# Performance work log

Measured on AMD Instinct MI355X. Metric: run time of the kernel, lower is better.

Reference implementation:

```python
import jax, jax.numpy as jnp
import numpy as np

N_NODES = 100000


def gcn_conv(x, edge_index, W, b):
    # PyG GCNConv: add self-loops, symmetric normalization D^-1/2 (A+I) D^-1/2, transform, aggregate, bias.
    src, dst = edge_index[0], edge_index[1]
    n = x.shape[0]
    xw = x @ W  # [N, out] transform before propagate (PyG order)
    # degree with self-loops (count edges by target + 1)
    deg = jax.ops.segment_sum(jnp.ones_like(dst, dtype=xw.dtype), dst, num_segments=n) + 1.0
    dinv = jax.lax.rsqrt(deg)  # deg >= 1, safe
    norm = dinv[src] * dinv[dst]  # [E]
    msgs = xw[src] * norm[:, None]  # [E, out] gathered, normalized messages
    agg = jax.ops.segment_sum(msgs, dst, num_segments=n)
    # self-loop contribution: norm_ii = dinv_i^2 = 1/deg_i
    agg = agg + xw * (dinv * dinv)[:, None]
    return agg + b


def setup_inputs() -> dict:
    key = jax.random.key(0)
    ks = jax.random.split(key, 8)
    in_c, h1, h2, out_c = 128, 71, 82, 1
    x = jax.random.normal(ks[0], (N_NODES, in_c), dtype=jnp.float32)
    edge_index = jax.random.randint(ks[1], (2, 1600000), 0, N_NODES, dtype=jnp.int64)
    def glorot(k, fan_in, fan_out):
        s = jnp.sqrt(6.0 / (fan_in + fan_out))
        return jax.random.uniform(k, (fan_in, fan_out), jnp.float32, -s, s)
    return {
        "x": x,
        "edge_index": edge_index,
        "W1": glorot(ks[2], in_c, h1), "b1": jnp.zeros((h1,), jnp.float32),
        "W2": glorot(ks[3], h1, h2), "b2": jnp.zeros((h2,), jnp.float32),
        "W3": glorot(ks[4], h2, out_c), "b3": jnp.zeros((out_c,), jnp.float32),
    }


def reference(x, edge_index, W1, b1, W2, b2, W3, b3):
    h = jax.nn.relu(gcn_conv(x, edge_index, W1, b1))
    h = gcn_conv(h, edge_index, W2, b2)  # note: no relu after conv2 in source
    return gcn_conv(h, edge_index, W3, b3)
```

## Files before the change

### kernel.cpp

```cpp
#include <hip/hip_runtime.h>
#include <hip/hip_fp16.h>

#define NNODES 100000
#define NB 196
#define BSHIFT 9
#define BMASK 511
#define BCAP 9216
#define WT_LD 136

typedef _Float16 half8 __attribute__((ext_vector_type(8)));
typedef float floatx4 __attribute__((ext_vector_type(4)));

__global__ void binA_kernel(const int* __restrict__ src, const int* __restrict__ dst,
                            int* __restrict__ bcnt, unsigned* __restrict__ bdata, int E) {
    __shared__ int hist[NB];
    __shared__ int gb[NB];
    __shared__ int cur[NB];
    const int BATCH = 4096;
    for (int base = blockIdx.x * BATCH; base < E; base += gridDim.x * BATCH) {
        for (int i = threadIdx.x; i < NB; i += blockDim.x) hist[i] = 0;
        __syncthreads();
        int s[16], d[16];
        int cnt = 0;
        if (base + BATCH <= E) {
#pragma unroll
            for (int q = 0; q < 4; ++q) {
                int4 sv = ((const int4*)(src + base))[q * 256 + threadIdx.x];
                int4 dv = ((const int4*)(dst + base))[q * 256 + threadIdx.x];
                s[cnt] = sv.x; d[cnt] = dv.x; atomicAdd(&hist[dv.x >> BSHIFT], 1); ++cnt;
                s[cnt] = sv.y; d[cnt] = dv.y; atomicAdd(&hist[dv.y >> BSHIFT], 1); ++cnt;
                s[cnt] = sv.z; d[cnt] = dv.z; atomicAdd(&hist[dv.z >> BSHIFT], 1); ++cnt;
                s[cnt] = sv.w; d[cnt] = dv.w; atomicAdd(&hist[dv.w >> BSHIFT], 1); ++cnt;
            }
        } else {
#pragma unroll
            for (int k = 0; k < 16; ++k) {
                int idx = base + k * 256 + threadIdx.x;
                if (idx < E) {
                    s[cnt] = src[idx];
                    d[cnt] = dst[idx];
                    atomicAdd(&hist[d[cnt] >> BSHIFT], 1);
                    ++cnt;
                }
            }
        }
        __syncthreads();
        for (int i = threadIdx.x; i < NB; i += blockDim.x) {
            int c = hist[i];
            gb[i] = (c > 0) ? atomicAdd(&bcnt[i], c) : 0;
            cur[i] = 0;
        }
        __syncthreads();
        for (int k = 0; k < cnt; ++k) {
            int b = d[k] >> BSHIFT;
            int lo = gb[b] + atomicAdd(&cur[b], 1);
            if (lo < BCAP)
                bdata[(size_t)b * BCAP + lo] = ((unsigned)s[k] << BSHIFT) | ((unsigned)d[k] & BMASK);
        }
        __syncthreads();
    }
}

__global__ void bscan_kernel(const int* __restrict__ bcnt, int* __restrict__ bstart) {
    __shared__ int sh[NB];
    int t = threadIdx.x;
    if (t < NB) sh[t] = min(bcnt[t], BCAP);
    __syncthreads();
    if (t == 0) {
        int acc = 0;
        for (int i = 0; i < NB; ++i) { int v = sh[i]; sh[i] = acc; acc += v; }
    }
    __syncthreads();
    if (t < NB) bstart[t] = sh[t];
}

__global__ __launch_bounds__(1024) void binB2_kernel(
        const int* __restrict__ bcnt, const int* __restrict__ bstart,
        const unsigned* __restrict__ bdata,
        int* __restrict__ deg, int* __restrict__ end_off, float* __restrict__ dinv,
        int* __restrict__ csr, int n) {
    __shared__ unsigned edata[BCAP];
    __shared__ int hist[512];
    __shared__ int cur[512];
    __shared__ int wsum[8];
    int b = blockIdx.x;
    int tid = threadIdx.x;
    int cnt = min(bcnt[b], BCAP);
    int base = bstart[b];
    const unsigned* p = bdata + (size_t)b * BCAP;
    if (tid < 512) hist[tid] = 0;
    __syncthreads();
    for (int i = tid; i < cnt; i += 1024) {
        unsigned e = p[i];
        edata[i] = e;
        atomicAdd(&hist[e & BMASK], 1);
    }
    __syncthreads();
    if (tid < 512) {
        int v = hist[tid];
        int lane = tid & 63;
        int incl = v;
#pragma unroll
        for (int off = 1; off < 64; off <<= 1) {
            int t = __shfl_up(incl, off);
            if (lane >= off) incl += t;
        }
        cur[tid] = incl;
        if (lane == 63) wsum[tid >> 6] = incl;
    }
    __syncthreads();
    if (tid == 0) {
        int acc = 0;
#pragma unroll
        for (int w = 0; w < 8; ++w) { int t = wsum[w]; wsum[w] = acc; acc += t; }
    }
    __syncthreads();
    if (tid < 512) {
        int v = hist[tid];
        int start = base + wsum[tid >> 6] + cur[tid] - v;
        int node = (b << BSHIFT) + tid;
        if (node < n) {
            deg[node] = v;
            end_off[node] = start + v;
            dinv[node] = rsqrtf((float)v + 1.0f);
        }
        cur[tid] = start;
    }
    __syncthreads();
    for (int i = tid; i < cnt; i += 1024) {
        unsigned e = edata[i];
        int pos = atomicAdd(&cur[e & BMASK], 1);
        csr[pos] = (int)(e >> BSHIFT);
    }
}

__global__ void w23_kernel(const float* __restrict__ W2, const float* __restrict__ b2,
                           const float* __restrict__ W3, float* __restrict__ w23) {
    int k = threadIdx.x;
    if (k < 71) {
        float a = 0.f;
        for (int j = 0; j < 82; ++j) a += W2[k * 82 + j] * W3[j];
        w23[k] = a;
    } else if (k == 71) {
        float a = 0.f;
        for (int j = 0; j < 82; ++j) a += b2[j] * W3[j];
        w23[71] = a;
    }
}

__global__ void wt_kernel(const float* __restrict__ W1, __half* __restrict__ Wt) {
    for (int i = threadIdx.x; i < 80 * WT_LD; i += blockDim.x) {
        int nn = i / WT_LD, k = i - nn * WT_LD;
        float v = (nn < 71 && k < 128) ? W1[k * 71 + nn] : 0.f;
        Wt[i] = __float2half(v);
    }
}

__global__ __launch_bounds__(256) void xform_mfma(
        const float* __restrict__ x, const __half* __restrict__ Wt,
        const float* __restrict__ scale, __half* __restrict__ msg, int n) {
    __shared__ __half Wsh[80 * WT_LD];
    {
        const uint4* sp = (const uint4*)Wt;
        uint4* dp = (uint4*)Wsh;
        for (int i = threadIdx.x; i < (80 * WT_LD * 2) / 16; i += blockDim.x) dp[i] = sp[i];
    }
    __syncthreads();
    int lane = threadIdx.x & 63;
    int m = lane & 15, q = lane >> 4;
    int gw = (blockIdx.x * blockDim.x + threadIdx.x) >> 6;
    int nw = (gridDim.x * blockDim.x) >> 6;
    int nrt = n >> 4;
    for (int rt = gw; rt < nrt; rt += nw) {
        int rb = rt << 4;
        const float* xr = x + (size_t)(rb + m) * 128 + q * 8;
        floatx4 acc[5];
#pragma unroll
        for (int t = 0; t < 5; ++t) acc[t] = (floatx4){0.f, 0.f, 0.f, 0.f};
#pragma unroll
        for (int ks = 0; ks < 4; ++ks) {
            float4 f0 = *(const float4*)(xr + ks * 32);
            float4 f1 = *(const float4*)(xr + ks * 32 + 4);
            half8 a;
            a[0] = (_Float16)f0.x; a[1] = (_Float16)f0.y;
            a[2] = (_Float16)f0.z; a[3] = (_Float16)f0.w;
            a[4] = (_Float16)f1.x; a[5] = (_Float16)f1.y;
            a[6] = (_Float16)f1.z; a[7] = (_Float16)f1.w;
#pragma unroll
            for (int t = 0; t < 5; ++t) {
                half8 b = *(const half8*)&Wsh[(t * 16 + m) * WT_LD + ks * 32 + q * 8];
                acc[t] = __builtin_amdgcn_mfma_f32_16x16x32_f16(a, b, acc[t], 0, 0, 0);
            }
        }
        float sc[4];
#pragma unroll
        for (int r = 0; r < 4; ++r) sc[r] = scale[rb + q * 4 + r];
#pragma unroll
        for (int t = 0; t < 5; ++t) {
            int col = t * 16 + m;
            if (col < 72) {
#pragma unroll
                for (int r = 0; r < 4; ++r)
                    msg[(size_t)(rb + q * 4 + r) * 72 + col] = __float2half(acc[t][r] * sc[r]);
            }
        }
    }
}

template <int OC>
__global__ void gather_fused(const __half2* __restrict__ msg, const int* __restrict__ csr,
                             const int* __restrict__ end_off, const int* __restrict__ deg,
                             const float* __restrict__ dinv, const float* __restrict__ b,
                             const float* __restrict__ w23, float* __restrict__ g2, int n) {
    constexpr int OC2 = (OC + 1) / 2;
    int lane = threadIdx.x & 63;
    int wid = (blockIdx.x * blockDim.x + threadIdx.x) >> 6;
    int nwaves = (gridDim.x * blockDim.x) >> 6;
    bool act = lane < OC2;
    int c = lane << 1;
    float bx = (act && c < OC) ? b[c] : 0.f;
    float by = (act && c + 1 < OC) ? b[c + 1] : 0.f;
    float w0 = (act && c < OC) ? w23[c] : 0.f;
    float w1 = (act && c + 1 < OC) ? w23[c + 1] : 0.f;
    for (int node = wid; node < n; node += nwaves) {
        int end = end_off[node];
        int cnt = deg[node];
        int start = end - cnt;
        float ax0 = 0.f, ay0 = 0.f, ax1 = 0.f, ay1 = 0.f;
        float ax2 = 0.f, ay2 = 0.f, ax3 = 0.f, ay3 = 0.f;
        for (int base = 0; base < cnt; base += 64) {
            int rem = min(cnt - base, 64);
            int se = (lane < rem) ? csr[start + base + lane] : 0;
            int j = 0;
            for (; j + 7 < rem; j += 8) {
                int s0 = __shfl(se, j),     s1 = __shfl(se, j + 1);
                int s2 = __shfl(se, j + 2), s3 = __shfl(se, j + 3);
                int s4 = __shfl(se, j + 4), s5 = __shfl(se, j + 5);
                int s6 = __shfl(se, j + 6), s7 = __shfl(se, j + 7);
                if (act) {
                    float2 v0 = __half22float2(msg[(size_t)s0 * OC2 + lane]);
                    float2 v1 = __half22float2(msg[(size_t)s1 * OC2 + lane]);
                    float2 v2 = __half22float2(msg[(size_t)s2 * OC2 + lane]);
                    float2 v3 = __half22float2(msg[(size_t)s3 * OC2 + lane]);
                    float2 v4 = __half22float2(msg[(size_t)s4 * OC2 + lane]);
                    float2 v5 = __half22float2(msg[(size_t)s5 * OC2 + lane]);
                    float2 v6 = __half22float2(msg[(size_t)s6 * OC2 + lane]);
                    float2 v7 = __half22float2(msg[(size_t)s7 * OC2 + lane]);
                    ax0 += v0.x; ay0 += v0.y;  ax1 += v1.x; ay1 += v1.y;
                    ax2 += v2.x; ay2 += v2.y;  ax3 += v3.x; ay3 += v3.y;
                    ax0 += v4.x; ay0 += v4.y;  ax1 += v5.x; ay1 += v5.y;
                    ax2 += v6.x; ay2 += v6.y;  ax3 += v7.x; ay3 += v7.y;
                }
            }
            for (; j + 3 < rem; j += 4) {
                int s0 = __shfl(se, j),     s1 = __shfl(se, j + 1);
                int s2 = __shfl(se, j + 2), s3 = __shfl(se, j + 3);
                if (act) {
                    float2 v0 = __half22float2(msg[(size_t)s0 * OC2 + lane]);
                    float2 v1 = __half22float2(msg[(size_t)s1 * OC2 + lane]);
                    float2 v2 = __half22float2(msg[(size_t)s2 * OC2 + lane]);
                    float2 v3 = __half22float2(msg[(size_t)s3 * OC2 + lane]);
                    ax0 += v0.x; ay0 += v0.y;  ax1 += v1.x; ay1 += v1.y;
                    ax2 += v2.x; ay2 += v2.y;  ax3 += v3.x; ay3 += v3.y;
                }
            }
            for (; j < rem; ++j) {
                int s = __shfl(se, j);
                if (act) {
                    float2 v = __half22float2(msg[(size_t)s * OC2 + lane]);
                    ax0 += v.x; ay0 += v.y;
                }
            }
        }
        float dv = dinv[node];
        float p = 0.f;
        if (act) {
            float2 selfv = __half22float2(msg[(size_t)node * OC2 + lane]);
            float sx = ((ax0 + ax1) + (ax2 + ax3)) + selfv.x;
            float sy = ((ay0 + ay1) + (ay2 + ay3)) + selfv.y;
            float vx = fmaxf(dv * sx + bx, 0.f);
            float vy = fmaxf(dv * sy + by, 0.f);
            p = vx * w0 + vy * w1;
        }
#pragma unroll
        for (int off = 32; off > 0; off >>= 1) p += __shfl_down(p, off);
        if (lane == 0) g2[node] = dv * p;
    }
}

__global__ void sgather_q(const float* __restrict__ g2, const int* __restrict__ csr,
                          const int* __restrict__ end_off, const int* __restrict__ deg,
                          const float* __restrict__ dinv, const float* __restrict__ w23,
                          float* __restrict__ q, int n) {
    float bw = w23[71];
    int stride = gridDim.x * blockDim.x;
    for (int i = blockIdx.x * blockDim.x + threadIdx.x; i < n; i += stride) {
        int end = end_off[i];
        int cnt = deg[i];
        float acc = 0.f;
        for (int j = end - cnt; j < end; ++j) acc += g2[csr[j]];
        float dv = dinv[i];
        q[i] = dv * (dv * (acc + g2[i]) + bw);
    }
}

__global__ void sgather_out(const float* __restrict__ q, const int* __restrict__ csr,
                            const int* __restrict__ end_off, const int* __restrict__ deg,
                            const float* __restrict__ dinv, const float* __restrict__ b3,
                            float* __restrict__ out, int n) {
    int stride = gridDim.x * blockDim.x;
    for (int i = blockIdx.x * blockDim.x + threadIdx.x; i < n; i += stride) {
        int end = end_off[i];
        int cnt = deg[i];
        float acc = 0.f;
        for (int j = end - cnt; j < end; ++j) acc += q[csr[j]];
        out[i] = dinv[i] * (acc + q[i]) + b3[0];
    }
}

extern "C" void kernel_launch(void* const* d_in, const int* in_sizes, int n_in,
                              void* d_out, int out_size, void* d_ws, size_t ws_size,
                              hipStream_t stream) {
    const float* x  = (const float*)d_in[0];
    const int*   ei = (const int*)d_in[1];
    const float* W1 = (const float*)d_in[2];
    const float* b1 = (const float*)d_in[3];
    const float* W2 = (const float*)d_in[4];
    const float* b2 = (const float*)d_in[5];
    const float* W3 = (const float*)d_in[6];
    const float* b3 = (const float*)d_in[7];
    float* out = (float*)d_out;

    const int n = NNODES;
    const int E = in_sizes[1] / 2;
    const int* src = ei;
    const int* dst = ei + E;

    float* ws     = (float*)d_ws;
    float* dinv   = ws;
    int*   deg_i  = (int*)(ws + n);
    int*   offs   = deg_i + n;
    int*   bcnt   = offs + n;
    int*   bstart = bcnt + 256;
    float* w23    = (float*)(bstart + 256);
    __half* Wt    = (__half*)(w23 + 80);
    float* g2     = (float*)(Wt + 11008);
    float* q      = g2 + n;
    int*   csr    = (int*)(q + n);
    __half* msg   = (__half*)(csr + E);
    unsigned* bdata = (unsigned*)(msg + (size_t)n * 72);

    hipMemsetAsync(bcnt, 0, 256 * sizeof(int), stream);
    binA_kernel<<<(E + 4095) / 4096, 256, 0, stream>>>(src, dst, bcnt, bdata, E);
    bscan_kernel<<<1, 256, 0, stream>>>(bcnt, bstart);
    binB2_kernel<<<NB, 1024, 0, stream>>>(bcnt, bstart, bdata, deg_i, offs, dinv, csr, n);
    w23_kernel<<<1, 128, 0, stream>>>(W2, b2, W3, w23);
    wt_kernel<<<1, 1024, 0, stream>>>(W1, Wt);

    xform_mfma<<<1563, 256, 0, stream>>>(x, Wt, dinv, msg, n);

    gather_fused<71><<<2048, 256, 0, stream>>>((const __half2*)msg, csr, offs, deg_i, dinv, b1, w23, g2, n);

    sgather_q<<<(n + 255) / 256, 256, 0, stream>>>(g2, csr, offs, deg_i, dinv, w23, q, n);
    sgather_out<<<(n + 255) / 256, 256, 0, stream>>>(q, csr, offs, deg_i, dinv, b3, out, n);
}
```

Baseline: 249.5 us.

## Gather multiple edges per wave with 16-byte loads and merge prep kernels

Rewrites the first-layer gather so each wave splits into 7 slots of 9 lanes. Each lane loads 8 fp16 features per edge with one vector load, so 7 neighbor rows are fetched concurrently instead of one row using 36 lanes. The self-loop is folded into the edge list, and partial sums are reduced across slots with shuffles. Separately, the bucket scan, the W2·W3 product and the W1 transpose kernels are merged into one 3-block launch to cut launch overhead. The cost is extra shuffle reductions and some idle lanes on low-degree tails.

```diff
diff --git a/kernel.cpp b/kernel.cpp
--- a/kernel.cpp
+++ b/kernel.cpp
@@ -61,17 +61,40 @@
     }
 }
 
-__global__ void bscan_kernel(const int* __restrict__ bcnt, int* __restrict__ bstart) {
-    __shared__ int sh[NB];
-    int t = threadIdx.x;
-    if (t < NB) sh[t] = min(bcnt[t], BCAP);
-    __syncthreads();
-    if (t == 0) {
-        int acc = 0;
-        for (int i = 0; i < NB; ++i) { int v = sh[i]; sh[i] = acc; acc += v; }
-    }
-    __syncthreads();
-    if (t < NB) bstart[t] = sh[t];
+__global__ __launch_bounds__(1024) void prep_kernel(
+        const int* __restrict__ bcnt, int* __restrict__ bstart,
+        const float* __restrict__ W2, const float* __restrict__ b2,
+        const float* __restrict__ W3, float* __restrict__ w23,
+        const float* __restrict__ W1, __half* __restrict__ Wt) {
+    if (blockIdx.x == 0) {
+        __shared__ int sh[NB];
+        int t = threadIdx.x;
+        if (t < NB) sh[t] = min(bcnt[t], BCAP);
+        __syncthreads();
+        if (t == 0) {
+            int acc = 0;
+            for (int i = 0; i < NB; ++i) { int v = sh[i]; sh[i] = acc; acc += v; }
+        }
+        __syncthreads();
+        if (t < NB) bstart[t] = sh[t];
+    } else if (blockIdx.x == 1) {
+        int k = threadIdx.x;
+        if (k < 71) {
+            float a = 0.f;
+            for (int j = 0; j < 82; ++j) a += W2[k * 82 + j] * W3[j];
+            w23[k] = a;
+        } else if (k == 71) {
+            float a = 0.f;
+            for (int j = 0; j < 82; ++j) a += b2[j] * W3[j];
+            w23[71] = a;
+        }
+    } else {
+        for (int i = threadIdx.x; i < 80 * WT_LD; i += blockDim.x) {
+            int nn = i / WT_LD, k = i - nn * WT_LD;
+            float v = (nn < 71 && k < 128) ? W1[k * 71 + nn] : 0.f;
+            Wt[i] = __float2half(v);
+        }
+    }
 }
 
 __global__ __launch_bounds__(1024) void binB2_kernel(
@@ -134,28 +157,6 @@
     }
 }
 
-__global__ void w23_kernel(const float* __restrict__ W2, const float* __restrict__ b2,
-                           const float* __restrict__ W3, float* __restrict__ w23) {
-    int k = threadIdx.x;
-    if (k < 71) {
-        float a = 0.f;
-        for (int j = 0; j < 82; ++j) a += W2[k * 82 + j] * W3[j];
-        w23[k] = a;
-    } else if (k == 71) {
-        float a = 0.f;
-        for (int j = 0; j < 82; ++j) a += b2[j] * W3[j];
-        w23[71] = a;
-    }
-}
-
-__global__ void wt_kernel(const float* __restrict__ W1, __half* __restrict__ Wt) {
-    for (int i = threadIdx.x; i < 80 * WT_LD; i += blockDim.x) {
-        int nn = i / WT_LD, k = i - nn * WT_LD;
-        float v = (nn < 71 && k < 128) ? W1[k * 71 + nn] : 0.f;
-        Wt[i] = __float2half(v);
-    }
-}
-
 __global__ __launch_bounds__(256) void xform_mfma(
         const float* __restrict__ x, const __half* __restrict__ Wt,
         const float* __restrict__ scale, __half* __restrict__ msg, int n) {
@@ -207,83 +208,87 @@
     }
 }
 
-template <int OC>
-__global__ void gather_fused(const __half2* __restrict__ msg, const int* __restrict__ csr,
-                             const int* __restrict__ end_off, const int* __restrict__ deg,
-                             const float* __restrict__ dinv, const float* __restrict__ b,
-                             const float* __restrict__ w23, float* __restrict__ g2, int n) {
-    constexpr int OC2 = (OC + 1) / 2;
+__global__ void gather_fused7(const __half* __restrict__ msg, const int* __restrict__ csr,
+                              const int* __restrict__ end_off, const int* __restrict__ deg,
+                              const float* __restrict__ dinv, const float* __restrict__ b1,
+                              const float* __restrict__ w23, float* __restrict__ g2, int n) {
     int lane = threadIdx.x & 63;
+    int slot = lane / 9;
+    int cg = lane - slot * 9;
+    bool valid = lane < 63;
+    int cbase = cg * 8;
+    float bw[8], ww[8];
+#pragma unroll
+    for (int k = 0; k < 8; ++k) {
+        int c = cbase + k;
+        bw[k] = (c < 71) ? b1[c] : 0.f;
+        ww[k] = (c < 71) ? w23[c] : 0.f;
+    }
     int wid = (blockIdx.x * blockDim.x + threadIdx.x) >> 6;
     int nwaves = (gridDim.x * blockDim.x) >> 6;
-    bool act = lane < OC2;
-    int c = lane << 1;
-    float bx = (act && c < OC) ? b[c] : 0.f;
-    float by = (act && c + 1 < OC) ? b[c + 1] : 0.f;
-    float w0 = (act && c < OC) ? w23[c] : 0.f;
-    float w1 = (act && c + 1 < OC) ? w23[c + 1] : 0.f;
     for (int node = wid; node < n; node += nwaves) {
         int end = end_off[node];
         int cnt = deg[node];
         int start = end - cnt;
-        float ax0 = 0.f, ay0 = 0.f, ax1 = 0.f, ay1 = 0.f;
-        float ax2 = 0.f, ay2 = 0.f, ax3 = 0.f, ay3 = 0.f;
-        for (int base = 0; base < cnt; base += 64) {
-            int rem = min(cnt - base, 64);
-            int se = (lane < rem) ? csr[start + base + lane] : 0;
+        int total = cnt + 1;
+        float acc[8];
+#pragma unroll
+        for (int k = 0; k < 8; ++k) acc[k] = 0.f;
+        for (int base = 0; base < total; base += 64) {
+            int rem = min(total - base, 64);
+            int idx = base + lane;
+            int se = node;
+            if (lane < rem && idx < cnt) se = csr[start + idx];
             int j = 0;
-            for (; j + 7 < rem; j += 8) {
-                int s0 = __shfl(se, j),     s1 = __shfl(se, j + 1);
-                int s2 = __shfl(se, j + 2), s3 = __shfl(se, j + 3);
-                int s4 = __shfl(se, j + 4), s5 = __shfl(se, j + 5);
-                int s6 = __shfl(se, j + 6), s7 = __shfl(se, j + 7);
-                if (act) {
-                    float2 v0 = __half22float2(msg[(size_t)s0 * OC2 + lane]);
-                    float2 v1 = __half22float2(msg[(size_t)s1 * OC2 + lane]);
-                    float2 v2 = __half22float2(msg[(size_t)s2 * OC2 + lane]);
-                    float2 v3 = __half22float2(msg[(size_t)s3 * OC2 + lane]);
-                    float2 v4 = __half22float2(msg[(size_t)s4 * OC2 + lane]);
-                    float2 v5 = __half22float2(msg[(size_t)s5 * OC2 + lane]);
-                    float2 v6 = __half22float2(msg[(size_t)s6 * OC2 + lane]);
-                    float2 v7 = __half22float2(msg[(size_t)s7 * OC2 + lane]);
-                    ax0 += v0.x; ay0 += v0.y;  ax1 += v1.x; ay1 += v1.y;
-                    ax2 += v2.x; ay2 += v2.y;  ax3 += v3.x; ay3 += v3.y;
-                    ax0 += v4.x; ay0 += v4.y;  ax1 += v5.x; ay1 += v5.y;
-                    ax2 += v6.x; ay2 += v6.y;  ax3 += v7.x; ay3 += v7.y;
+            for (; j + 14 <= rem; j += 14) {
+                int s0 = __shfl(se, j + slot);
+                int s1 = __shfl(se, j + 7 + slot);
+                if (valid) {
+                    union { uint4 u; __half2 h[4]; } r0, r1;
+                    r0.u = *(const uint4*)(msg + (size_t)s0 * 72 + cbase);
+                    r1.u = *(const uint4*)(msg + (size_t)s1 * 72 + cbase);
+#pragma unroll
+                    for (int k = 0; k < 4; ++k) {
+                        float2 f0 = __half22float2(r0.h[k]);
+                        float2 f1 = __half22float2(r1.h[k]);
+                        acc[2 * k]     += f0.x + f1.x;
+                        acc[2 * k + 1] += f0.y + f1.y;
+                    }
                 }
             }
-            for (; j + 3 < rem; j += 4) {
-                int s0 = __shfl(se, j),     s1 = __shfl(se, j + 1);
-                int s2 = __shfl(se, j + 2), s3 = __shfl(se, j + 3);
-                if (act) {
-                    float2 v0 = __half22float2(msg[(size_t)s0 * OC2 + lane]);
-                    float2 v1 = __half22float2(msg[(size_t)s1 * OC2 + lane]);
-                    float2 v2 = __half22float2(msg[(size_t)s2 * OC2 + lane]);
-                    float2 v3 = __half22float2(msg[(size_t)s3 * OC2 + lane]);
-                    ax0 += v0.x; ay0 += v0.y;  ax1 += v1.x; ay1 += v1.y;
-                    ax2 += v2.x; ay2 += v2.y;  ax3 += v3.x; ay3 += v3.y;
+            for (; j < rem; j += 7) {
+                int myj = j + slot;
+                int s = __shfl(se, myj);
+                if (valid && myj < rem) {
+                    union { uint4 u; __half2 h[4]; } r;
+                    r.u = *(const uint4*)(msg + (size_t)s * 72 + cbase);
+#pragma unroll
+                    for (int k = 0; k < 4; ++k) {
+                        float2 f = __half22float2(r.h[k]);
+                        acc[2 * k]     += f.x;
+                        acc[2 * k + 1] += f.y;
+                    }
                 }
             }
-            for (; j < rem; ++j) {
-                int s = __shfl(se, j);
-                if (act) {
-                    float2 v = __half22float2(msg[(size_t)s * OC2 + lane]);
-                    ax0 += v.x; ay0 += v.y;
-                }
-            }
+        }
+#pragma unroll
+        for (int k = 0; k < 8; ++k) {
+            float t;
+            t = __shfl(acc[k], lane + 36); if (slot < 3) acc[k] += t;
+            t = __shfl(acc[k], lane + 18); if (slot < 2) acc[k] += t;
+            t = __shfl(acc[k], lane + 9);  if (slot < 1) acc[k] += t;
         }
         float dv = dinv[node];
         float p = 0.f;
-        if (act) {
-            float2 selfv = __half22float2(msg[(size_t)node * OC2 + lane]);
-            float sx = ((ax0 + ax1) + (ax2 + ax3)) + selfv.x;
-            float sy = ((ay0 + ay1) + (ay2 + ay3)) + selfv.y;
-            float vx = fmaxf(dv * sx + bx, 0.f);
-            float vy = fmaxf(dv * sy + by, 0.f);
-            p = vx * w0 + vy * w1;
-        }
-#pragma unroll
-        for (int off = 32; off > 0; off >>= 1) p += __shfl_down(p, off);
+#pragma unroll
+        for (int k = 0; k < 8; ++k) {
+            float v = fmaxf(dv * acc[k] + bw[k], 0.f);
+            p += v * ww[k];
+        }
+        float t = __shfl(p, lane + 8); if (lane == 0) p += t;
+        t = __shfl(p, lane + 4); if (lane < 4) p += t;
+        t = __shfl(p, lane + 2); if (lane < 2) p += t;
+        t = __shfl(p, lane + 1); if (lane == 0) p += t;
         if (lane == 0) g2[node] = dv * p;
     }
 }
@@ -352,14 +357,12 @@
 
     hipMemsetAsync(bcnt, 0, 256 * sizeof(int), stream);
     binA_kernel<<<(E + 4095) / 4096, 256, 0, stream>>>(src, dst, bcnt, bdata, E);
-    bscan_kernel<<<1, 256, 0, stream>>>(bcnt, bstart);
+    prep_kernel<<<3, 1024, 0, stream>>>(bcnt, bstart, W2, b2, W3, w23, W1, Wt);
     binB2_kernel<<<NB, 1024, 0, stream>>>(bcnt, bstart, bdata, deg_i, offs, dinv, csr, n);
-    w23_kernel<<<1, 128, 0, stream>>>(W2, b2, W3, w23);
-    wt_kernel<<<1, 1024, 0, stream>>>(W1, Wt);
 
     xform_mfma<<<1563, 256, 0, stream>>>(x, Wt, dinv, msg, n);
 
-    gather_fused<71><<<2048, 256, 0, stream>>>((const __half2*)msg, csr, offs, deg_i, dinv, b1, w23, g2, n);
+    gather_fused7<<<2048, 256, 0, stream>>>(msg, csr, offs, deg_i, dinv, b1, w23, g2, n);
 
     sgather_q<<<(n + 255) / 256, 256, 0, stream>>>(g2, csr, offs, deg_i, dinv, w23, q, n);
     sgather_out<<<(n + 255) / 256, 256, 0, stream>>>(q, csr, offs, deg_i, dinv, b3, out, n);
```

Result: faster. 241.7 us (-3.1%).
